# Kernel tuning notes

Measured on AMD Instinct MI355X. Metric: run time of the kernel, lower is better.

The kernel has to match this reference:

```python
import jax, jax.numpy as jnp
import numpy as np

COLB = 16            # COL_BLOCK_WIDTH
IN_W = 1024          # input_width; zero_inputs=0 so input_locations = arange(IN_W)
OUT_W = 512          # output_width
DEPTH = 8            # network_depth
IN_L = 4             # butterfly_in_depth
OUT_L = 4            # butterfly_out_depth
ACT = 8              # activations_per_block
BLOCKS = 64          # blocks_per_layer -> num_inputs = 1024 per module
CURV = 1.0
GROW = BLOCKS * ACT  # 512 new rows per module
TOTAL = IN_W + DEPTH * GROW  # 5120
BATCH = 4096


def setup_inputs() -> dict:
    key = jax.random.key(0)
    k1, k2, k3 = jax.random.split(key, 3)
    input_data = jax.random.normal(k1, (IN_W, BATCH), dtype=jnp.float32)
    scales = jnp.full((IN_W,), 0.05, dtype=jnp.float32)
    # angles uniform in (-pi, pi), shape [depth, in_layers+out_layers, num_inputs/2]
    angles = (jax.random.uniform(k2, (DEPTH, IN_L + OUT_L, BLOCKS * COLB // 2)) * 2.0 - 1.0) * np.pi
    angles = angles.astype(jnp.float32)
    biases = jax.random.normal(k3, (DEPTH, GROW), dtype=jnp.float32) * 0.05
    # per-module indices_in = randperm(total_width_so_far)[:num_inputs]
    rng = np.random.RandomState(0)
    tw = IN_W
    idxs = []
    for _ in range(DEPTH):
        idxs.append(rng.permutation(tw)[: BLOCKS * COLB].astype(np.int32))
        tw += GROW
    indices_in = jnp.asarray(np.stack(idxs))  # [depth, 1024]
    return {"input_data": input_data, "scales": scales, "angles": angles,
            "biases": biases, "indices_in": indices_in}


def _rotate(x, ang, stride):
    # x: [W, B]; pair row i (with (i//stride)%2==0) with row i+stride inside 16-blocks
    W, B = x.shape
    xr = x.reshape(W // (2 * stride), 2, stride, B)
    a = ang.reshape(W // (2 * stride), stride)[:, :, None]
    c, s = jnp.cos(a), jnp.sin(a)
    lo, hi = xr[:, 0], xr[:, 1]              # [W/2s, s, B]
    nlo = c * lo + s * hi
    nhi = -s * lo + c * hi
    return jnp.stack([nlo, nhi], axis=1).reshape(W, B)


def _butterfly_module(data, ang, bias, idx, idx_out):
    W = BLOCKS * COLB
    x = data[idx]                             # gather [1024, B]
    for l in range(IN_L):
        x = _rotate(x, ang[l], 2 ** (l % 4))
    xb = x.reshape(BLOCKS, COLB, -1)
    pre = xb[:, :ACT, :] + bias.reshape(BLOCKS, ACT)[:, :, None]
    # curvature (smoothed-ReLU) activation
    act = 0.5 * (pre + jnp.sqrt(pre * pre + CURV * CURV))
    xb = xb.at[:, :ACT, :].set(act)
    x = xb.reshape(W, -1)
    for l in range(OUT_L):
        x = _rotate(x, ang[IN_L + l], 2 ** ((IN_L + l) % 4))
    data = data.at[idx].set(x)                # scatter working set back
    data = data.at[idx_out: idx_out + GROW].set(act.reshape(GROW, -1))
    return data


def reference(input_data, scales, angles, biases, indices_in):
    B = input_data.shape[1]
    data = jnp.zeros((TOTAL, B), dtype=input_data.dtype)
    data = data.at[:IN_W].set(scales[:, None] * input_data)
    for i in range(DEPTH):
        data = _butterfly_module(data, angles[i], biases[i], indices_in[i], IN_W + GROW * i)
    return data[TOTAL - OUT_W:]
```

## Files before the change

### kernel.cpp

```cpp
#include <hip/hip_runtime.h>
#include <math.h>

#define N_INW     1024
#define N_DEPTH   8
#define N_GROW    512
#define N_BATCH   4096
#define N_THREADS 128
#define N_LAYERS  64

typedef __attribute__((ext_vector_type(2))) float F2;
typedef decltype(__builtin_amdgcn_cvt_pkrtz(0.f, 0.f)) H2;

__global__ void precompute_cs_kernel(const float* __restrict__ angles,
                                     float* __restrict__ cs) {
    int i = blockIdx.x * blockDim.x + threadIdx.x;
    if (i < N_LAYERS * 512) {
        int g = i >> 9, p = i & 511;
        float a = angles[i];
        cs[(2 * g) * 512 + p]     = cosf(a);
        cs[(2 * g + 1) * 512 + p] = sinf(a);
    }
}

#define ADDR(r) (((r) << 3) + ((((r) >> 4)) << 2) + cpo)

#define LD2(A) ({ H2 _h = *(const H2*)(L + (A));                               \
                  F2 _v; _v.x = (float)_h.x; _v.y = (float)_h.y; _v; })
#define ST2(A, V) do { F2 _w = (V);                                            \
    *(H2*)(L + (A)) = __builtin_amdgcn_cvt_pkrtz(_w.x, _w.y); } while (0)

#define LDCS(g, CA, CB, SA, SB) do { if (USE_TABLE) {                          \
    const float4* _c = (const float4*)(cs_tab + (2*(g))*512 + (blk<<3));       \
    const float4* _s = (const float4*)(cs_tab + (2*(g)+1)*512 + (blk<<3));     \
    CA = _c[0]; CB = _c[1]; SA = _s[0]; SB = _s[1];                            \
  } else {                                                                     \
    const float4* _p = (const float4*)(angles + (g)*512 + (blk<<3));           \
    float4 _a = _p[0], _b = _p[1];                                             \
    __sincosf(_a.x, &SA.x, &CA.x); __sincosf(_a.y, &SA.y, &CA.y);              \
    __sincosf(_a.z, &SA.z, &CA.z); __sincosf(_a.w, &SA.w, &CA.w);              \
    __sincosf(_b.x, &SB.x, &CB.x); __sincosf(_b.y, &SB.y, &CB.y);              \
    __sincosf(_b.z, &SB.z, &CB.z); __sincosf(_b.w, &SB.w, &CB.w);              \
  } } while (0)

#define ROTP(LO, HI, CC, SS) do { F2 _l = LO, _h = HI;                         \
    LO = CC * _l + SS * _h; HI = CC * _h - SS * _l; } while (0)

#define ROTS1(CA,CB,SA,SB) do {                                                \
    ROTP(x0,x1,CA.x,SA.x);  ROTP(x2,x3,CA.y,SA.y);                             \
    ROTP(x4,x5,CA.z,SA.z);  ROTP(x6,x7,CA.w,SA.w);                             \
    ROTP(x8,x9,CB.x,SB.x);  ROTP(x10,x11,CB.y,SB.y);                           \
    ROTP(x12,x13,CB.z,SB.z);ROTP(x14,x15,CB.w,SB.w); } while (0)
#define ROTS2(CA,CB,SA,SB) do {                                                \
    ROTP(x0,x2,CA.x,SA.x);  ROTP(x1,x3,CA.y,SA.y);                             \
    ROTP(x4,x6,CA.z,SA.z);  ROTP(x5,x7,CA.w,SA.w);                             \
    ROTP(x8,x10,CB.x,SB.x); ROTP(x9,x11,CB.y,SB.y);                            \
    ROTP(x12,x14,CB.z,SB.z);ROTP(x13,x15,CB.w,SB.w); } while (0)
#define ROTS4(CA,CB,SA,SB) do {                                                \
    ROTP(x0,x4,CA.x,SA.x);  ROTP(x1,x5,CA.y,SA.y);                             \
    ROTP(x2,x6,CA.z,SA.z);  ROTP(x3,x7,CA.w,SA.w);                             \
    ROTP(x8,x12,CB.x,SB.x); ROTP(x9,x13,CB.y,SB.y);                            \
    ROTP(x10,x14,CB.z,SB.z);ROTP(x11,x15,CB.w,SB.w); } while (0)
#define ROTS8(CA,CB,SA,SB) do {                                                \
    ROTP(x0,x8,CA.x,SA.x);  ROTP(x1,x9,CA.y,SA.y);                             \
    ROTP(x2,x10,CA.z,SA.z); ROTP(x3,x11,CA.w,SA.w);                            \
    ROTP(x4,x12,CB.x,SB.x); ROTP(x5,x13,CB.y,SB.y);                            \
    ROTP(x6,x14,CB.z,SB.z); ROTP(x7,x15,CB.w,SB.w); } while (0)

#define ACT1(X, BB) do { F2 _p = (X) + (BB);                                   \
    F2 _t = _p * _p + 1.0f;                                                    \
    F2 _r; _r.x = __builtin_amdgcn_sqrtf(_t.x);                                \
    _r.y = __builtin_amdgcn_sqrtf(_t.y);                                       \
    X = 0.5f * (_p + _r); } while (0)

#define FENCE() __builtin_amdgcn_sched_barrier(0)

#define MODULE(M) {                                                            \
  const int a0=ADDR(i0.x), a1=ADDR(i0.y), a2=ADDR(i0.z), a3=ADDR(i0.w),        \
            a4=ADDR(i1.x), a5=ADDR(i1.y), a6=ADDR(i1.z), a7=ADDR(i1.w),        \
            a8=ADDR(i2.x), a9=ADDR(i2.y), a10=ADDR(i2.z), a11=ADDR(i2.w),      \
            a12=ADDR(i3.x), a13=ADDR(i3.y), a14=ADDR(i3.z), a15=ADDR(i3.w);    \
              \
  F2 x0=LD2(a0), x1=LD2(a1), x2=LD2(a2), x3=LD2(a3);                           \
  F2 x4=LD2(a4), x5=LD2(a5), x6=LD2(a6), x7=LD2(a7);                           \
  F2 x8=LD2(a8), x9=LD2(a9), x10=LD2(a10), x11=LD2(a11);                       \
  F2 x12=LD2(a12), x13=LD2(a13), x14=LD2(a14), x15=LD2(a15);                   \
  float4 da0,db0,ta0,tb0, da1,db1,ta1,tb1, da2,db2,ta2,tb2, da3,db3,ta3,tb3;   \
  if ((M) < 7) {                                                               \
    LDCS(8*(M)+4, da0,db0,ta0,tb0);                                            \
    LDCS(8*(M)+5, da1,db1,ta1,tb1);                                            \
    LDCS(8*(M)+6, da2,db2,ta2,tb2);                                            \
    LDCS(8*(M)+7, da3,db3,ta3,tb3);                                            \
  }                                                                            \
  FENCE();                                                                     \
                      \
  ROTS1(ca0,cb0,sa0,sb0);                                                      \
  ROTS2(ca1,cb1,sa1,sb1);                                                      \
  ROTS4(ca2,cb2,sa2,sb2);                                                      \
  ROTS8(ca3,cb3,sa3,sb3);                                                      \
  ACT1(x0,bA.x); ACT1(x1,bA.y); ACT1(x2,bA.z); ACT1(x3,bA.w);                  \
  ACT1(x4,bB.x); ACT1(x5,bB.y); ACT1(x6,bB.z); ACT1(x7,bB.w);                  \
  if ((M) < 7) {                                                               \
                                                          \
    const int _br = N_INW + (M)*N_GROW + (blk<<3);                             \
    const int _ab = ADDR(_br);                                                 \
    ST2(_ab+ 0,x0); ST2(_ab+ 8,x1); ST2(_ab+16,x2); ST2(_ab+24,x3);            \
    ST2(_ab+32,x4); ST2(_ab+40,x5); ST2(_ab+48,x6); ST2(_ab+56,x7);            \
                 \
    LDCS(8*(M)+8,  ca0,cb0,sa0,sb0);                                           \
    LDCS(8*(M)+9,  ca1,cb1,sa1,sb1);                                           \
    LDCS(8*(M)+10, ca2,cb2,sa2,sb2);                                           \
    LDCS(8*(M)+11, ca3,cb3,sa3,sb3);                                           \
    { const int4* _ip = (const int4*)(indices + ((M)+1)*N_INW + (blk<<4));     \
      i0=_ip[0]; i1=_ip[1]; i2=_ip[2]; i3=_ip[3]; }                            \
    { const float4* _bp = (const float4*)(biases + ((M)+1)*N_GROW + (blk<<3)); \
      bA = _bp[0]; bB = _bp[1]; }                                              \
    FENCE();                                                                   \
                         \
    ROTS1(da0,db0,ta0,tb0);                                                    \
    ROTS2(da1,db1,ta1,tb1);                                                    \
    ROTS4(da2,db2,ta2,tb2);                                                    \
    ROTS8(da3,db3,ta3,tb3);                                                    \
    ST2(a0,x0);  ST2(a1,x1);  ST2(a2,x2);  ST2(a3,x3);                         \
    ST2(a4,x4);  ST2(a5,x5);  ST2(a6,x6);  ST2(a7,x7);                         \
    ST2(a8,x8);  ST2(a9,x9);  ST2(a10,x10); ST2(a11,x11);                      \
    ST2(a12,x12); ST2(a13,x13); ST2(a14,x14); ST2(a15,x15);                    \
  } else {                                                                     \
        \
    *(F2*)(out + (size_t)((blk<<3)+0)*N_BATCH + cg) = x0;                      \
    *(F2*)(out + (size_t)((blk<<3)+1)*N_BATCH + cg) = x1;                      \
    *(F2*)(out + (size_t)((blk<<3)+2)*N_BATCH + cg) = x2;                      \
    *(F2*)(out + (size_t)((blk<<3)+3)*N_BATCH + cg) = x3;                      \
    *(F2*)(out + (size_t)((blk<<3)+4)*N_BATCH + cg) = x4;                      \
    *(F2*)(out + (size_t)((blk<<3)+5)*N_BATCH + cg) = x5;                      \
    *(F2*)(out + (size_t)((blk<<3)+6)*N_BATCH + cg) = x6;                      \
    *(F2*)(out + (size_t)((blk<<3)+7)*N_BATCH + cg) = x7;                      \
  } }

template <bool USE_TABLE>
__global__ __launch_bounds__(N_THREADS, 2)
void butterfly_fused_kernel(const float* __restrict__ input,
                            const float* __restrict__ scales,
                            const float* __restrict__ biases,
                            const int*   __restrict__ indices,
                            const float* __restrict__ cs_tab,
                            const float* __restrict__ angles,
                            float* __restrict__ out) {
    extern __shared__ float ldsbuf[];
    char* L = (char*)ldsbuf;
    const int t   = threadIdx.x;
    const int blk = t & 63;
    const int cp  = t >> 6;
    const int cpo = cp << 2;
    const int b   = blockIdx.x;
    const int cg  = ((((b & 7) * 128) + (b >> 3)) << 2) + (cp << 1);

    float4 ca0,cb0,sa0,sb0, ca1,cb1,sa1,sb1, ca2,cb2,sa2,sb2, ca3,cb3,sa3,sb3;
    float4 bA, bB;
    int4 i0, i1, i2, i3;

    { const int4* ip = (const int4*)(indices + (blk << 4));
      i0 = ip[0]; i1 = ip[1]; i2 = ip[2]; i3 = ip[3]; }
    LDCS(0, ca0,cb0,sa0,sb0);
    LDCS(1, ca1,cb1,sa1,sb1);
    LDCS(2, ca2,cb2,sa2,sb2);
    LDCS(3, ca3,cb3,sa3,sb3);
    { const float4* bp = (const float4*)(biases + (blk << 3));
      bA = bp[0]; bB = bp[1]; }

#pragma unroll
    for (int k = 0; k < 16; ++k) {
        const int r = (k << 6) + blk;
        F2 v = *(const F2*)(input + (size_t)r * N_BATCH + cg);
        ST2(ADDR(r), scales[r] * v);
    }

    MODULE(0) MODULE(1) MODULE(2) MODULE(3)
    MODULE(4) MODULE(5) MODULE(6) MODULE(7)
}

extern "C" void kernel_launch(void* const* d_in, const int* in_sizes, int n_in,
                              void* d_out, int out_size, void* d_ws, size_t ws_size,
                              hipStream_t stream) {
    const float* input   = (const float*)d_in[0];
    const float* scales  = (const float*)d_in[1];
    const float* angles  = (const float*)d_in[2];
    const float* biases  = (const float*)d_in[3];
    const int*   indices = (const int*)d_in[4];
    float* out = (float*)d_out;

    const size_t cs_bytes  = (size_t)N_LAYERS * 2 * 512 * sizeof(float);
    const size_t lds_bytes = (size_t)288 * 132;
    const int grid = N_BATCH / 4;

    if (ws_size >= cs_bytes) {
        precompute_cs_kernel<<<N_LAYERS * 512 / 256, 256, 0, stream>>>(angles, (float*)d_ws);
        butterfly_fused_kernel<true><<<grid, N_THREADS, lds_bytes, stream>>>(
            input, scales, biases, indices, (const float*)d_ws, angles, out);
    } else {
        butterfly_fused_kernel<false><<<grid, N_THREADS, lds_bytes, stream>>>(
            input, scales, biases, indices, nullptr, angles, out);
    }
}
```

Baseline: 103.3 us.

## Use one wave per block with two columns and precomputed LDS addresses

Each block drops from 128 to 64 threads, so every block handles one column pair (2 batch columns) and the grid doubles to 2048 blocks, with a matching smaller LDS layout. Gather indices are turned into LDS byte offsets ahead of time in the precompute kernel and stored in the workspace, which takes the per-row address arithmetic out of the main kernel. The aim is to lower per-block LDS use and raise occupancy while removing integer work. The cost is more blocks, each redoing the same loads of indices, angle tables and biases, and an extra workspace table.

```diff
diff --git a/kernel.cpp b/kernel.cpp
--- a/kernel.cpp
+++ b/kernel.cpp
@@ -5,14 +5,16 @@
 #define N_DEPTH   8
 #define N_GROW    512
 #define N_BATCH   4096
-#define N_THREADS 128
+#define N_THREADS 64
 #define N_LAYERS  64
 
 typedef __attribute__((ext_vector_type(2))) float F2;
 typedef decltype(__builtin_amdgcn_cvt_pkrtz(0.f, 0.f)) H2;
 
-__global__ void precompute_cs_kernel(const float* __restrict__ angles,
-                                     float* __restrict__ cs) {
+__global__ void precompute_kernel(const float* __restrict__ angles,
+                                  const int*   __restrict__ indices,
+                                  float* __restrict__ cs,
+                                  int*   __restrict__ addrs) {
     int i = blockIdx.x * blockDim.x + threadIdx.x;
     if (i < N_LAYERS * 512) {
         int g = i >> 9, p = i & 511;
@@ -20,9 +22,13 @@
         cs[(2 * g) * 512 + p]     = cosf(a);
         cs[(2 * g + 1) * 512 + p] = sinf(a);
     }
+    if (i < N_DEPTH * N_INW) {
+        int v = indices[i];
+        addrs[i] = (v + (v >> 4)) << 2;
+    }
 }
 
-#define ADDR(r) (((r) << 3) + ((((r) >> 4)) << 2) + cpo)
+#define ADDR(r) ((((r) + ((r) >> 4))) << 2)
 
 #define LD2(A) ({ H2 _h = *(const H2*)(L + (A));                               \
                   F2 _v; _v.x = (float)_h.x; _v.y = (float)_h.y; _v; })
@@ -40,6 +46,19 @@
     __sincosf(_a.z, &SA.z, &CA.z); __sincosf(_a.w, &SA.w, &CA.w);              \
     __sincosf(_b.x, &SB.x, &CB.x); __sincosf(_b.y, &SB.y, &CB.y);              \
     __sincosf(_b.z, &SB.z, &CB.z); __sincosf(_b.w, &SB.w, &CB.w);              \
+  } } while (0)
+
+#define TR(v) (((v) + ((v) >> 4)) << 2)
+#define LDADDR(m) do { if (USE_TABLE) {                                        \
+    const int4* _ip = (const int4*)(addr_tab + (m)*N_INW + (blk<<4));          \
+    i0 = _ip[0]; i1 = _ip[1]; i2 = _ip[2]; i3 = _ip[3];                        \
+  } else {                                                                     \
+    const int4* _ip = (const int4*)(indices + (m)*N_INW + (blk<<4));           \
+    int4 _v0=_ip[0], _v1=_ip[1], _v2=_ip[2], _v3=_ip[3];                       \
+    i0.x=TR(_v0.x); i0.y=TR(_v0.y); i0.z=TR(_v0.z); i0.w=TR(_v0.w);            \
+    i1.x=TR(_v1.x); i1.y=TR(_v1.y); i1.z=TR(_v1.z); i1.w=TR(_v1.w);            \
+    i2.x=TR(_v2.x); i2.y=TR(_v2.y); i2.z=TR(_v2.z); i2.w=TR(_v2.w);            \
+    i3.x=TR(_v3.x); i3.y=TR(_v3.y); i3.z=TR(_v3.z); i3.w=TR(_v3.w);            \
   } } while (0)
 
 #define ROTP(LO, HI, CC, SS) do { F2 _l = LO, _h = HI;                         \
@@ -75,10 +94,9 @@
 #define FENCE() __builtin_amdgcn_sched_barrier(0)
 
 #define MODULE(M) {                                                            \
-  const int a0=ADDR(i0.x), a1=ADDR(i0.y), a2=ADDR(i0.z), a3=ADDR(i0.w),        \
-            a4=ADDR(i1.x), a5=ADDR(i1.y), a6=ADDR(i1.z), a7=ADDR(i1.w),        \
-            a8=ADDR(i2.x), a9=ADDR(i2.y), a10=ADDR(i2.z), a11=ADDR(i2.w),      \
-            a12=ADDR(i3.x), a13=ADDR(i3.y), a14=ADDR(i3.z), a15=ADDR(i3.w);    \
+  const int a0=i0.x, a1=i0.y, a2=i0.z, a3=i0.w, a4=i1.x, a5=i1.y,              \
+            a6=i1.z, a7=i1.w, a8=i2.x, a9=i2.y, a10=i2.z, a11=i2.w,            \
+            a12=i3.x, a13=i3.y, a14=i3.z, a15=i3.w;                            \
               \
   F2 x0=LD2(a0), x1=LD2(a1), x2=LD2(a2), x3=LD2(a3);                           \
   F2 x4=LD2(a4), x5=LD2(a5), x6=LD2(a6), x7=LD2(a7);                           \
@@ -103,15 +121,14 @@
                                                           \
     const int _br = N_INW + (M)*N_GROW + (blk<<3);                             \
     const int _ab = ADDR(_br);                                                 \
-    ST2(_ab+ 0,x0); ST2(_ab+ 8,x1); ST2(_ab+16,x2); ST2(_ab+24,x3);            \
-    ST2(_ab+32,x4); ST2(_ab+40,x5); ST2(_ab+48,x6); ST2(_ab+56,x7);            \
-                 \
+    ST2(_ab+ 0,x0); ST2(_ab+ 4,x1); ST2(_ab+ 8,x2); ST2(_ab+12,x3);            \
+    ST2(_ab+16,x4); ST2(_ab+20,x5); ST2(_ab+24,x6); ST2(_ab+28,x7);            \
+        \
     LDCS(8*(M)+8,  ca0,cb0,sa0,sb0);                                           \
     LDCS(8*(M)+9,  ca1,cb1,sa1,sb1);                                           \
     LDCS(8*(M)+10, ca2,cb2,sa2,sb2);                                           \
     LDCS(8*(M)+11, ca3,cb3,sa3,sb3);                                           \
-    { const int4* _ip = (const int4*)(indices + ((M)+1)*N_INW + (blk<<4));     \
-      i0=_ip[0]; i1=_ip[1]; i2=_ip[2]; i3=_ip[3]; }                            \
+    LDADDR((M)+1);                                                             \
     { const float4* _bp = (const float4*)(biases + ((M)+1)*N_GROW + (blk<<3)); \
       bA = _bp[0]; bB = _bp[1]; }                                              \
     FENCE();                                                                   \
@@ -143,23 +160,20 @@
                             const float* __restrict__ biases,
                             const int*   __restrict__ indices,
                             const float* __restrict__ cs_tab,
+                            const int*   __restrict__ addr_tab,
                             const float* __restrict__ angles,
                             float* __restrict__ out) {
     extern __shared__ float ldsbuf[];
     char* L = (char*)ldsbuf;
-    const int t   = threadIdx.x;
-    const int blk = t & 63;
-    const int cp  = t >> 6;
-    const int cpo = cp << 2;
+    const int blk = threadIdx.x;
     const int b   = blockIdx.x;
-    const int cg  = ((((b & 7) * 128) + (b >> 3)) << 2) + (cp << 1);
+    const int cg  = (((b & 7) * 256) + (b >> 3)) * 2;
 
     float4 ca0,cb0,sa0,sb0, ca1,cb1,sa1,sb1, ca2,cb2,sa2,sb2, ca3,cb3,sa3,sb3;
     float4 bA, bB;
     int4 i0, i1, i2, i3;
 
-    { const int4* ip = (const int4*)(indices + (blk << 4));
-      i0 = ip[0]; i1 = ip[1]; i2 = ip[2]; i3 = ip[3]; }
+    LDADDR(0);
     LDCS(0, ca0,cb0,sa0,sb0);
     LDCS(1, ca1,cb1,sa1,sb1);
     LDCS(2, ca2,cb2,sa2,sb2);
@@ -189,15 +203,18 @@
     float* out = (float*)d_out;
 
     const size_t cs_bytes  = (size_t)N_LAYERS * 2 * 512 * sizeof(float);
-    const size_t lds_bytes = (size_t)288 * 132;
-    const int grid = N_BATCH / 4;
-
-    if (ws_size >= cs_bytes) {
-        precompute_cs_kernel<<<N_LAYERS * 512 / 256, 256, 0, stream>>>(angles, (float*)d_ws);
+    const size_t adr_bytes = (size_t)N_DEPTH * N_INW * sizeof(int);
+    const size_t lds_bytes = (size_t)4608 * 4 + 288 * 4;
+    const int grid = N_BATCH / 2;
+
+    if (ws_size >= cs_bytes + adr_bytes) {
+        float* cs  = (float*)d_ws;
+        int* addrs = (int*)((char*)d_ws + cs_bytes);
+        precompute_kernel<<<N_LAYERS * 512 / 256, 256, 0, stream>>>(angles, indices, cs, addrs);
         butterfly_fused_kernel<true><<<grid, N_THREADS, lds_bytes, stream>>>(
-            input, scales, biases, indices, (const float*)d_ws, angles, out);
+            input, scales, biases, indices, cs, addrs, angles, out);
     } else {
         butterfly_fused_kernel<false><<<grid, N_THREADS, lds_bytes, stream>>>(
-            input, scales, biases, indices, nullptr, angles, out);
+            input, scales, biases, indices, nullptr, nullptr, angles, out);
     }
 }
```

Result: no change. 103.0 us (-0.3%).
